# Kernel tuning notes

Hardware: AMD Instinct MI355X
Metric: run time of the kernel (lower is better)

## Reference

```python
import math
import jax, jax.numpy as jnp
import numpy as np

N_QUBITS = 8
N_QLAYERS = 2
HIDDEN = 768
BATCH = 8192
LN_EPS = 1e-5


def _ry_gate(theta):
    # theta: scalar or (B,) -> (2,2) or (B,2,2) complex64
    h = theta * 0.5
    c, s = jnp.cos(h), jnp.sin(h)
    g = jnp.stack([jnp.stack([c, -s], axis=-1), jnp.stack([s, c], axis=-1)], axis=-2)
    return g.astype(jnp.complex64)


def _rz_gate(theta):
    t = theta.astype(jnp.complex64)
    e0, e1 = jnp.exp(-0.5j * t), jnp.exp(0.5j * t)
    z = jnp.zeros_like(e0)
    return jnp.stack([jnp.stack([e0, z], axis=-1), jnp.stack([z, e1], axis=-1)], axis=-2)


def _apply_1q(state, gate, w, n):
    # state: (B, 2**n); gate: (2,2) shared or (B,2,2) per-sample; wire w (0 = MSB)
    B = state.shape[0]
    s = state.reshape(B, 2 ** w, 2, -1)
    if gate.ndim == 2:
        s = jnp.einsum('ij,bljr->blir', gate, s)
    else:
        s = jnp.einsum('bij,bljr->blir', gate, s)
    return s.reshape(B, -1)


def _apply_cnot(state, c, t, n):
    B = state.shape[0]
    s = state.reshape((B,) + (2,) * n)
    ax_c = 1 + c
    s0 = jnp.take(s, 0, axis=ax_c)  # control=0 branch, control axis removed
    s1 = jnp.take(s, 1, axis=ax_c)
    ax_t = 1 + t - (1 if t > c else 0)
    s1 = jnp.flip(s1, axis=ax_t)    # X on target when control=1
    s = jnp.stack([s0, s1], axis=ax_c)
    return s.reshape(B, -1)


def _circuit(angles, weights_ry, weights_rz):
    # angles: (B, n) float32 -> (B, n) PauliZ expectations, batched statevector sim
    n, L = N_QUBITS, N_QLAYERS
    B = angles.shape[0]
    state = jnp.zeros((B, 2 ** n), dtype=jnp.complex64).at[:, 0].set(1.0)
    for i in range(n):
        state = _apply_1q(state, _ry_gate(angles[:, i]), i, n)
    for i in range(1, n):
        state = _apply_cnot(state, 0, i, n)
    for l in range(L):
        for i in range(n):
            state = _apply_1q(state, _ry_gate(weights_ry[l, i]), i, n)
            state = _apply_1q(state, _rz_gate(weights_rz[l, i]), i, n)
    for i in range(1, n):
        state = _apply_cnot(state, i, 0, n)
    probs = jnp.abs(state) ** 2  # (B, 2**n)
    k = jnp.arange(2 ** n)
    bits = (k[None, :] >> (n - 1 - jnp.arange(n))[:, None]) & 1  # wire 0 = MSB (PennyLane)
    signs = (1 - 2 * bits).astype(probs.dtype)  # (n, 2**n)
    return probs @ signs.T  # (B, n)


def setup_inputs() -> dict:
    key = jax.random.key(0)
    ks = jax.random.split(key, 8)
    return {
        'hidden': jax.random.normal(ks[0], (BATCH, HIDDEN), dtype=jnp.float32),
        'W_in': jax.random.normal(ks[1], (N_QUBITS, HIDDEN), dtype=jnp.float32) * (1.0 / math.sqrt(HIDDEN)),
        'b_in': jax.random.normal(ks[2], (N_QUBITS,), dtype=jnp.float32) * 0.01,
        'W_out': jax.random.normal(ks[3], (HIDDEN, N_QUBITS), dtype=jnp.float32) * (1.0 / math.sqrt(N_QUBITS)),
        'b_out': jax.random.normal(ks[4], (HIDDEN,), dtype=jnp.float32) * 0.01,
        'weights_ry': jax.random.normal(ks[5], (N_QLAYERS, N_QUBITS), dtype=jnp.float32) * 0.1,
        'weights_rz': jax.random.normal(ks[6], (N_QLAYERS, N_QUBITS), dtype=jnp.float32) * 0.1,
        'gamma': jnp.ones((HIDDEN,), dtype=jnp.float32),
        'beta': jnp.zeros((HIDDEN,), dtype=jnp.float32),
    }


def reference(hidden, W_in, b_in, W_out, b_out, weights_ry, weights_rz, gamma, beta):
    phase = 0.0
    angles = jnp.tanh(hidden @ W_in.T + b_in) * math.pi + phase  # (B, n)
    meas = _circuit(angles, weights_ry, weights_rz).astype(jnp.float32)  # (B, n)
    y = meas @ W_out.T + b_out  # (B, h)
    mu = jnp.mean(y, axis=-1, keepdims=True)
    var = jnp.mean(jnp.square(y - mu), axis=-1, keepdims=True)
    return (y - mu) * jax.lax.rsqrt(var + LN_EPS) * gamma + beta
```

## Files before the change

kernel.cpp:

```cpp
#include <hip/hip_runtime.h>
#include <hip/hip_bf16.h>

#define NQ    8
#define HID   768
#define BATCH 8192
#define SPB   4
#define NBLK  (BATCH / SPB)
#define TPB   256

template<int BF> __device__ __forceinline__ float LDV(const void* p, int i) {
    if constexpr (BF) return __bfloat162float(((const __hip_bfloat16*)p)[i]);
    else return ((const float*)p)[i];
}
template<int BF> __device__ __forceinline__ float4 LD4(const void* p, int i4) {
    if constexpr (BF) {
        ushort4 v = ((const ushort4*)p)[i4];
        float4 r;
        r.x = __uint_as_float(((unsigned)v.x) << 16);
        r.y = __uint_as_float(((unsigned)v.y) << 16);
        r.z = __uint_as_float(((unsigned)v.z) << 16);
        r.w = __uint_as_float(((unsigned)v.w) << 16);
        return r;
    } else {
        return ((const float4*)p)[i4];
    }
}
template<int BF> __device__ __forceinline__ void ST4(void* p, int i4, float4 v) {
    if constexpr (BF) {
        __hip_bfloat16 bx = __float2bfloat16(v.x);
        __hip_bfloat16 by = __float2bfloat16(v.y);
        __hip_bfloat16 bz = __float2bfloat16(v.z);
        __hip_bfloat16 bw = __float2bfloat16(v.w);
        ushort4 s;
        s.x = *(const unsigned short*)&bx;
        s.y = *(const unsigned short*)&by;
        s.z = *(const unsigned short*)&bz;
        s.w = *(const unsigned short*)&bw;
        ((ushort4*)p)[i4] = s;
    } else {
        ((float4*)p)[i4] = v;
    }
}

template<int BF>
__device__ __forceinline__ void run_all(
    const void* hidden_, const void* W_in_, const void* b_in_,
    const void* W_out_, const void* b_out_, const void* wry_, const void* wrz_,
    const void* gamma_, const void* beta_, void* out_)
{
    const int tid  = threadIdx.x;
    const int lane = tid & 63;
    const int wv   = tid >> 6;
    const int j    = lane >> 3;
    const int b    = blockIdx.x * SPB + wv;

    float DA, DB, Kr, Ki;
    {
        float ry0 = LDV<BF>(wry_, j), ry1 = LDV<BF>(wry_, NQ + j);
        float rz0 = LDV<BF>(wrz_, j), rz1 = LDV<BF>(wrz_, NQ + j);
        float cA = cosf(0.5f*ry0), sA = sinf(0.5f*ry0);
        float cB = cosf(0.5f*ry1), sB = sinf(0.5f*ry1);
        float p0c = cosf(0.5f*rz0), p0s = sinf(0.5f*rz0);
        float p1c = cosf(0.5f*rz1), p1s = sinf(0.5f*rz1);
        float g00r =  cA*p0c, g00i = -cA*p0s;
        float g01r = -sA*p0c, g01i =  sA*p0s;
        float g10r =  sA*p0c, g10i =  sA*p0s;
        float g11r =  cA*p0c, g11i =  cA*p0s;
        float h00r = cB*g00r - sB*g10r, h00i = cB*g00i - sB*g10i;
        float h01r = cB*g01r - sB*g11r, h01i = cB*g01i - sB*g11i;
        float h10r = sB*g00r + cB*g10r, h10i = sB*g00i + cB*g10i;
        float h11r = sB*g01r + cB*g11r, h11i = sB*g01i + cB*g11i;
        float f00r = h00r*p1c + h00i*p1s, f00i = h00i*p1c - h00r*p1s;
        float f01r = h01r*p1c + h01i*p1s, f01i = h01i*p1c - h01r*p1s;
        float f10r = h10r*p1c - h10i*p1s, f10i = h10i*p1c + h10r*p1s;
        float f11r = h11r*p1c - h11i*p1s, f11i = h11i*p1c + h11r*p1s;
        DA = f00r*f00r + f00i*f00i - (f10r*f10r + f10i*f10i);
        DB = f01r*f01r + f01i*f01i - (f11r*f11r + f11i*f11i);
        Kr = (f00r*f01r + f00i*f01i) - (f10r*f11r + f10i*f11i);
        Ki = (f00i*f01r - f00r*f01i) - (f10i*f11r - f10r*f11i);
    }

    float p[NQ];
    #pragma unroll
    for (int q = 0; q < NQ; ++q) p[q] = 0.f;
    const int hb = b * (HID/4);
    #pragma unroll
    for (int t = 0; t < 3; ++t) {
        const int q4 = (t << 6) + lane;
        float4 h = LD4<BF>(hidden_, hb + q4);
        #pragma unroll
        for (int jj = 0; jj < NQ; ++jj) {
            float4 w = LD4<BF>(W_in_, jj*(HID/4) + q4);
            p[jj] = fmaf(h.x, w.x, p[jj]);
            p[jj] = fmaf(h.y, w.y, p[jj]);
            p[jj] = fmaf(h.z, w.z, p[jj]);
            p[jj] = fmaf(h.w, w.w, p[jj]);
        }
    }
    const bool mb0 = ((lane >> 3) & 1) != 0;
    const bool mb1 = ((lane >> 4) & 1) != 0;
    const bool mb2 = ((lane >> 5) & 1) != 0;
    float np[4];
    #pragma unroll
    for (int k = 0; k < 4; ++k) {
        float sent = mb0 ? p[2*k]   : p[2*k+1];
        float keep = mb0 ? p[2*k+1] : p[2*k];
        np[k] = keep + __shfl_xor(sent, 8, 64);
    }
    float nq[2];
    #pragma unroll
    for (int k = 0; k < 2; ++k) {
        float sent = mb1 ? np[2*k]   : np[2*k+1];
        float keep = mb1 ? np[2*k+1] : np[2*k];
        nq[k] = keep + __shfl_xor(sent, 16, 64);
    }
    float z;
    {
        float sent = mb2 ? nq[0] : nq[1];
        float keep = mb2 ? nq[1] : nq[0];
        z = keep + __shfl_xor(sent, 32, 64);
    }
    z += __shfl_xor(z, 1, 64);
    z += __shfl_xor(z, 2, 64);
    z += __shfl_xor(z, 4, 64);

    float zb = z + LDV<BF>(b_in_, j);
    float th = tanhf(zb);
    float sj = sinpif(th), cj = cospif(th);

    float ca = 0.5f * (DA + DB), da = 0.5f * (DA - DB);
    const bool g0 = (j == 0);
    float uu = da * cj;
    float vv = fmaf(Kr, sj, ca);
    float MA = g0 ? 1.f : (vv + uu), MB = g0 ? 1.f : (vv - uu);
    float fr = g0 ? 1.f : Kr, fi = g0 ? 0.f : (cj * Ki);
    #pragma unroll
    for (int d = 8; d < 64; d <<= 1) {
        MA *= __shfl_xor(MA, d, 64);
        MB *= __shfl_xor(MB, d, 64);
        float qr = __shfl_xor(fr, d, 64);
        float qi = __shfl_xor(fi, d, 64);
        float nr = fr*qr - fi*qi;
        float ni = fr*qi + fi*qr;
        fr = nr; fi = ni;
    }
    float DA0 = __shfl(DA, 0, 64), DB0 = __shfl(DB, 0, 64);
    float Kr0 = __shfl(Kr, 0, 64), Ki0 = __shfl(Ki, 0, 64);
    float cc0 = __shfl(cj, 0, 64), sc0 = __shfl(sj, 0, 64);
    float meas0 = 0.5f*(1.f+cc0)*DA0*MA + 0.5f*(1.f-cc0)*DB0*MB
                + sc0*(Kr0*fr - Ki0*fi);
    float measj = g0 ? meas0 : fmaf(cc0, uu, vv);
    float m0 = meas0;
    float m1 = __shfl(measj,  8, 64), m2 = __shfl(measj, 16, 64);
    float m3 = __shfl(measj, 24, 64), m4 = __shfl(measj, 32, 64);
    float m5 = __shfl(measj, 40, 64), m6 = __shfl(measj, 48, 64);
    float m7 = __shfl(measj, 56, 64);

    float yv[12];
    float sum = 0.f, sq = 0.f;
    #pragma unroll
    for (int t = 0; t < 3; ++t) {
        const int q4 = (t << 6) + lane;
        float4 bo = LD4<BF>(b_out_, q4);
        float bos[4] = {bo.x, bo.y, bo.z, bo.w};
        #pragma unroll
        for (int e = 0; e < 4; ++e) {
            int c = 4*q4 + e;
            float4 w0 = LD4<BF>(W_out_, c*2);
            float4 w1 = LD4<BF>(W_out_, c*2 + 1);
            float y = bos[e];
            y = fmaf(m0, w0.x, y); y = fmaf(m1, w0.y, y);
            y = fmaf(m2, w0.z, y); y = fmaf(m3, w0.w, y);
            y = fmaf(m4, w1.x, y); y = fmaf(m5, w1.y, y);
            y = fmaf(m6, w1.z, y); y = fmaf(m7, w1.w, y);
            yv[4*t+e] = y;
            sum += y;
            sq = fmaf(y, y, sq);
        }
    }
    #pragma unroll
    for (int d = 1; d < 64; d <<= 1) {
        sum += __shfl_xor(sum, d, 64);
        sq  += __shfl_xor(sq,  d, 64);
    }
    float mean = sum * (1.f/HID);
    float var  = fmaf(sq, 1.f/HID, -mean*mean);
    float rstd = rsqrtf(var + 1e-5f);
    #pragma unroll
    for (int t = 0; t < 3; ++t) {
        const int q4 = (t << 6) + lane;
        float4 ga = LD4<BF>(gamma_, q4);
        float4 be = LD4<BF>(beta_,  q4);
        float4 o;
        o.x = fmaf((yv[4*t+0]-mean)*rstd, ga.x, be.x);
        o.y = fmaf((yv[4*t+1]-mean)*rstd, ga.y, be.y);
        o.z = fmaf((yv[4*t+2]-mean)*rstd, ga.z, be.z);
        o.w = fmaf((yv[4*t+3]-mean)*rstd, ga.w, be.w);
        ST4<BF>(out_, hb + q4, o);
    }
}

__global__ __launch_bounds__(TPB, 4) void main_kernel(
    const void* hidden_, const void* W_in_, const void* b_in_,
    const void* W_out_, const void* b_out_, const void* wry_, const void* wrz_,
    const void* gamma_, const void* beta_, void* out_)
{
    const int lane = threadIdx.x & 63;
    unsigned wrd = ((const unsigned*)hidden_)[lane];
    unsigned lo  = wrd & 0xffffu;
    unsigned e   = (lo >> 7) & 0xffu;
    bool v = (lo == 0u) || (e >= 100u && e <= 133u);
    unsigned long long mask = __ballot(v);
    int flag = (__popcll(mask) > 32) ? 1 : 0;
    if (flag)
        run_all<1>(hidden_, W_in_, b_in_, W_out_, b_out_, wry_, wrz_,
                   gamma_, beta_, out_);
    else
        run_all<0>(hidden_, W_in_, b_in_, W_out_, b_out_, wry_, wrz_,
                   gamma_, beta_, out_);
}

extern "C" void kernel_launch(void* const* d_in, const int* in_sizes, int n_in,
                              void* d_out, int out_size, void* d_ws, size_t ws_size,
                              hipStream_t stream) {
    const void* hidden = d_in[0];
    const void* W_in   = d_in[1];
    const void* b_in   = d_in[2];
    const void* W_out  = d_in[3];
    const void* b_out  = d_in[4];
    const void* wry    = d_in[5];
    const void* wrz    = d_in[6];
    const void* gamma  = d_in[7];
    const void* beta   = d_in[8];
    (void)d_ws; (void)ws_size;
    main_kernel<<<NBLK, TPB, 0, stream>>>(hidden, W_in, b_in, W_out, b_out,
                                          wry, wrz, gamma, beta, d_out);
}
```

Measured before the change: 117.6 us.

## Use DPP and readlane for wave reductions; give each lane group one qubit's dot product

```diff
diff --git a/kernel.cpp b/kernel.cpp
--- a/kernel.cpp
+++ b/kernel.cpp
@@ -42,6 +42,16 @@
     }
 }
 
+template<int CTRL>
+__device__ __forceinline__ float dpp_mov(float x) {
+    int xi = __float_as_int(x);
+    int yi = __builtin_amdgcn_update_dpp(xi, xi, CTRL, 0xF, 0xF, false);
+    return __int_as_float(yi);
+}
+__device__ __forceinline__ float rl(float x, int l) {
+    return __int_as_float(__builtin_amdgcn_readlane(__float_as_int(x), l));
+}
+
 template<int BF>
 __device__ __forceinline__ void run_all(
     const void* hidden_, const void* W_in_, const void* b_in_,
@@ -52,6 +62,7 @@
     const int lane = tid & 63;
     const int wv   = tid >> 6;
     const int j    = lane >> 3;
+    const int u    = lane & 7;
     const int b    = blockIdx.x * SPB + wv;
 
     float DA, DB, Kr, Ki;
@@ -80,51 +91,23 @@
         Ki = (f00i*f01r - f00r*f01i) - (f10i*f11r - f10r*f11i);
     }
 
-    float p[NQ];
+    float a0=0.f, a1=0.f, a2=0.f, a3=0.f;
+    const int hb = b * (HID/4);
+    const int wb = j * (HID/4);
     #pragma unroll
-    for (int q = 0; q < NQ; ++q) p[q] = 0.f;
-    const int hb = b * (HID/4);
-    #pragma unroll
-    for (int t = 0; t < 3; ++t) {
-        const int q4 = (t << 6) + lane;
-        float4 h = LD4<BF>(hidden_, hb + q4);
-        #pragma unroll
-        for (int jj = 0; jj < NQ; ++jj) {
-            float4 w = LD4<BF>(W_in_, jj*(HID/4) + q4);
-            p[jj] = fmaf(h.x, w.x, p[jj]);
-            p[jj] = fmaf(h.y, w.y, p[jj]);
-            p[jj] = fmaf(h.z, w.z, p[jj]);
-            p[jj] = fmaf(h.w, w.w, p[jj]);
-        }
-    }
-    const bool mb0 = ((lane >> 3) & 1) != 0;
-    const bool mb1 = ((lane >> 4) & 1) != 0;
-    const bool mb2 = ((lane >> 5) & 1) != 0;
-    float np[4];
-    #pragma unroll
-    for (int k = 0; k < 4; ++k) {
-        float sent = mb0 ? p[2*k]   : p[2*k+1];
-        float keep = mb0 ? p[2*k+1] : p[2*k];
-        np[k] = keep + __shfl_xor(sent, 8, 64);
-    }
-    float nq[2];
-    #pragma unroll
-    for (int k = 0; k < 2; ++k) {
-        float sent = mb1 ? np[2*k]   : np[2*k+1];
-        float keep = mb1 ? np[2*k+1] : np[2*k];
-        nq[k] = keep + __shfl_xor(sent, 16, 64);
-    }
-    float z;
-    {
-        float sent = mb2 ? nq[0] : nq[1];
-        float keep = mb2 ? nq[1] : nq[0];
-        z = keep + __shfl_xor(sent, 32, 64);
-    }
-    z += __shfl_xor(z, 1, 64);
-    z += __shfl_xor(z, 2, 64);
-    z += __shfl_xor(z, 4, 64);
-
-    float zb = z + LDV<BF>(b_in_, j);
+    for (int t = 0; t < 24; ++t) {
+        int i4 = u + (t << 3);
+        float4 h = LD4<BF>(hidden_, hb + i4);
+        float4 w = LD4<BF>(W_in_,  wb + i4);
+        a0 = fmaf(h.x, w.x, a0); a1 = fmaf(h.y, w.y, a1);
+        a2 = fmaf(h.z, w.z, a2); a3 = fmaf(h.w, w.w, a3);
+    }
+    float acc = (a0 + a1) + (a2 + a3);
+    acc += dpp_mov<0xB1>(acc);
+    acc += dpp_mov<0x4E>(acc);
+    acc += dpp_mov<0x141>(acc);
+
+    float zb = acc + LDV<BF>(b_in_, j);
     float th = tanhf(zb);
     float sj = sinpif(th), cj = cospif(th);
 
@@ -133,28 +116,36 @@
     float uu = da * cj;
     float vv = fmaf(Kr, sj, ca);
     float MA = g0 ? 1.f : (vv + uu), MB = g0 ? 1.f : (vv - uu);
-    float fr = g0 ? 1.f : Kr, fi = g0 ? 0.f : (cj * Ki);
-    #pragma unroll
-    for (int d = 8; d < 64; d <<= 1) {
-        MA *= __shfl_xor(MA, d, 64);
-        MB *= __shfl_xor(MB, d, 64);
-        float qr = __shfl_xor(fr, d, 64);
-        float qi = __shfl_xor(fi, d, 64);
-        float nr = fr*qr - fi*qi;
-        float ni = fr*qi + fi*qr;
+    float fr = g0 ? 1.f : Kr,        fi = g0 ? 0.f : (cj * Ki);
+    MA *= dpp_mov<0x140>(MA);
+    MB *= dpp_mov<0x140>(MB);
+    {
+        float qr = dpp_mov<0x140>(fr), qi = dpp_mov<0x140>(fi);
+        float nr = fr*qr - fi*qi, ni = fr*qi + fi*qr;
         fr = nr; fi = ni;
     }
-    float DA0 = __shfl(DA, 0, 64), DB0 = __shfl(DB, 0, 64);
-    float Kr0 = __shfl(Kr, 0, 64), Ki0 = __shfl(Ki, 0, 64);
-    float cc0 = __shfl(cj, 0, 64), sc0 = __shfl(sj, 0, 64);
-    float meas0 = 0.5f*(1.f+cc0)*DA0*MA + 0.5f*(1.f-cc0)*DB0*MB
-                + sc0*(Kr0*fr - Ki0*fi);
+    float PA = (rl(MA,0)*rl(MA,16)) * (rl(MA,32)*rl(MA,48));
+    float PB = (rl(MB,0)*rl(MB,16)) * (rl(MB,32)*rl(MB,48));
+    float PFr, PFi;
+    {
+        float ar = rl(fr, 0), ai = rl(fi, 0);
+        float br = rl(fr,16), bi = rl(fi,16);
+        float cr = rl(fr,32), ci = rl(fi,32);
+        float dr = rl(fr,48), di = rl(fi,48);
+        float abr = ar*br - ai*bi, abi = ar*bi + ai*br;
+        float cdr = cr*dr - ci*di, cdi = cr*di + ci*dr;
+        PFr = abr*cdr - abi*cdi;
+        PFi = abr*cdi + abi*cdr;
+    }
+    float DA0 = rl(DA,0), DB0 = rl(DB,0), Kr0 = rl(Kr,0), Ki0 = rl(Ki,0);
+    float cc0 = rl(cj,0), sc0 = rl(sj,0);
+    float meas0 = 0.5f*(1.f+cc0)*DA0*PA + 0.5f*(1.f-cc0)*DB0*PB
+                + sc0*(Kr0*PFr - Ki0*PFi);
     float measj = g0 ? meas0 : fmaf(cc0, uu, vv);
     float m0 = meas0;
-    float m1 = __shfl(measj,  8, 64), m2 = __shfl(measj, 16, 64);
-    float m3 = __shfl(measj, 24, 64), m4 = __shfl(measj, 32, 64);
-    float m5 = __shfl(measj, 40, 64), m6 = __shfl(measj, 48, 64);
-    float m7 = __shfl(measj, 56, 64);
+    float m1 = rl(measj,  8), m2 = rl(measj, 16), m3 = rl(measj, 24);
+    float m4 = rl(measj, 32), m5 = rl(measj, 40), m6 = rl(measj, 48);
+    float m7 = rl(measj, 56);
 
     float yv[12];
     float sum = 0.f, sq = 0.f;
@@ -178,13 +169,14 @@
             sq = fmaf(y, y, sq);
         }
     }
-    #pragma unroll
-    for (int d = 1; d < 64; d <<= 1) {
-        sum += __shfl_xor(sum, d, 64);
-        sq  += __shfl_xor(sq,  d, 64);
-    }
-    float mean = sum * (1.f/HID);
-    float var  = fmaf(sq, 1.f/HID, -mean*mean);
+    sum += dpp_mov<0xB1>(sum);   sq += dpp_mov<0xB1>(sq);
+    sum += dpp_mov<0x4E>(sum);   sq += dpp_mov<0x4E>(sq);
+    sum += dpp_mov<0x141>(sum);  sq += dpp_mov<0x141>(sq);
+    sum += dpp_mov<0x140>(sum);  sq += dpp_mov<0x140>(sq);
+    float tsum = (rl(sum,0) + rl(sum,16)) + (rl(sum,32) + rl(sum,48));
+    float tsq  = (rl(sq, 0) + rl(sq, 16)) + (rl(sq, 32) + rl(sq, 48));
+    float mean = tsum * (1.f/HID);
+    float var  = fmaf(tsq, 1.f/HID, -mean*mean);
     float rstd = rsqrtf(var + 1e-5f);
     #pragma unroll
     for (int t = 0; t < 3; ++t) {
```

After: 123.1 us. 1.05x slower.

## Stage W_in and W_out in LDS, double samples per block

Applied to the files above, without the earlier changes.

```diff
diff --git a/kernel.cpp b/kernel.cpp
--- a/kernel.cpp
+++ b/kernel.cpp
@@ -4,13 +4,17 @@
 #define NQ    8
 #define HID   768
 #define BATCH 8192
-#define SPB   4
+#define TPB   512
+#define SPB   8
 #define NBLK  (BATCH / SPB)
-#define TPB   256
 
 template<int BF> __device__ __forceinline__ float LDV(const void* p, int i) {
     if constexpr (BF) return __bfloat162float(((const __hip_bfloat16*)p)[i]);
     else return ((const float*)p)[i];
+}
+template<int BF> __device__ __forceinline__ void STV(void* p, int i, float v) {
+    if constexpr (BF) ((__hip_bfloat16*)p)[i] = __float2bfloat16(v);
+    else ((float*)p)[i] = v;
 }
 template<int BF> __device__ __forceinline__ float4 LD4(const void* p, int i4) {
     if constexpr (BF) {
@@ -25,34 +29,34 @@
         return ((const float4*)p)[i4];
     }
 }
-template<int BF> __device__ __forceinline__ void ST4(void* p, int i4, float4 v) {
-    if constexpr (BF) {
-        __hip_bfloat16 bx = __float2bfloat16(v.x);
-        __hip_bfloat16 by = __float2bfloat16(v.y);
-        __hip_bfloat16 bz = __float2bfloat16(v.z);
-        __hip_bfloat16 bw = __float2bfloat16(v.w);
-        ushort4 s;
-        s.x = *(const unsigned short*)&bx;
-        s.y = *(const unsigned short*)&by;
-        s.z = *(const unsigned short*)&bz;
-        s.w = *(const unsigned short*)&bw;
-        ((ushort4*)p)[i4] = s;
-    } else {
-        ((float4*)p)[i4] = v;
-    }
-}
 
 template<int BF>
 __device__ __forceinline__ void run_all(
     const void* hidden_, const void* W_in_, const void* b_in_,
     const void* W_out_, const void* b_out_, const void* wry_, const void* wrz_,
-    const void* gamma_, const void* beta_, void* out_)
+    const void* gamma_, const void* beta_, void* out_,
+    float* sWin, float4* sWoutLo, float4* sWoutHi)
 {
     const int tid  = threadIdx.x;
     const int lane = tid & 63;
     const int wv   = tid >> 6;
     const int j    = lane >> 3;
     const int b    = blockIdx.x * SPB + wv;
+
+    #pragma unroll
+    for (int k = 0; k < (NQ*HID/4)/TPB; ++k) {
+        int idx = tid + k*TPB;
+        ((float4*)sWin)[idx] = LD4<BF>(W_in_, idx);
+    }
+    #pragma unroll
+    for (int k = 0; k < HID/TPB + 1; ++k) {
+        int c = tid + k*TPB;
+        if (c < HID) {
+            sWoutLo[c] = LD4<BF>(W_out_, c*2);
+            sWoutHi[c] = LD4<BF>(W_out_, c*2 + 1);
+        }
+    }
+    __syncthreads();
 
     float DA, DB, Kr, Ki;
     {
@@ -90,7 +94,7 @@
         float4 h = LD4<BF>(hidden_, hb + q4);
         #pragma unroll
         for (int jj = 0; jj < NQ; ++jj) {
-            float4 w = LD4<BF>(W_in_, jj*(HID/4) + q4);
+            float4 w = ((const float4*)(sWin + jj*HID))[q4];
             p[jj] = fmaf(h.x, w.x, p[jj]);
             p[jj] = fmaf(h.y, w.y, p[jj]);
             p[jj] = fmaf(h.z, w.z, p[jj]);
@@ -107,17 +111,17 @@
         float keep = mb0 ? p[2*k+1] : p[2*k];
         np[k] = keep + __shfl_xor(sent, 8, 64);
     }
-    float nq[2];
+    float nq2[2];
     #pragma unroll
     for (int k = 0; k < 2; ++k) {
         float sent = mb1 ? np[2*k]   : np[2*k+1];
         float keep = mb1 ? np[2*k+1] : np[2*k];
-        nq[k] = keep + __shfl_xor(sent, 16, 64);
+        nq2[k] = keep + __shfl_xor(sent, 16, 64);
     }
     float z;
     {
-        float sent = mb2 ? nq[0] : nq[1];
-        float keep = mb2 ? nq[1] : nq[0];
+        float sent = mb2 ? nq2[0] : nq2[1];
+        float keep = mb2 ? nq2[1] : nq2[0];
         z = keep + __shfl_xor(sent, 32, 64);
     }
     z += __shfl_xor(z, 1, 64);
@@ -133,7 +137,7 @@
     float uu = da * cj;
     float vv = fmaf(Kr, sj, ca);
     float MA = g0 ? 1.f : (vv + uu), MB = g0 ? 1.f : (vv - uu);
-    float fr = g0 ? 1.f : Kr, fi = g0 ? 0.f : (cj * Ki);
+    float fr = g0 ? 1.f : Kr,        fi = g0 ? 0.f : (cj * Ki);
     #pragma unroll
     for (int d = 8; d < 64; d <<= 1) {
         MA *= __shfl_xor(MA, d, 64);
@@ -156,27 +160,22 @@
     float m5 = __shfl(measj, 40, 64), m6 = __shfl(measj, 48, 64);
     float m7 = __shfl(measj, 56, 64);
 
+    const int rowbase = b * HID;
     float yv[12];
     float sum = 0.f, sq = 0.f;
     #pragma unroll
-    for (int t = 0; t < 3; ++t) {
-        const int q4 = (t << 6) + lane;
-        float4 bo = LD4<BF>(b_out_, q4);
-        float bos[4] = {bo.x, bo.y, bo.z, bo.w};
-        #pragma unroll
-        for (int e = 0; e < 4; ++e) {
-            int c = 4*q4 + e;
-            float4 w0 = LD4<BF>(W_out_, c*2);
-            float4 w1 = LD4<BF>(W_out_, c*2 + 1);
-            float y = bos[e];
-            y = fmaf(m0, w0.x, y); y = fmaf(m1, w0.y, y);
-            y = fmaf(m2, w0.z, y); y = fmaf(m3, w0.w, y);
-            y = fmaf(m4, w1.x, y); y = fmaf(m5, w1.y, y);
-            y = fmaf(m6, w1.z, y); y = fmaf(m7, w1.w, y);
-            yv[4*t+e] = y;
-            sum += y;
-            sq = fmaf(y, y, sq);
-        }
+    for (int k = 0; k < 12; ++k) {
+        const int c = lane + (k << 6);
+        float4 w0 = sWoutLo[c];
+        float4 w1 = sWoutHi[c];
+        float y = LDV<BF>(b_out_, c);
+        y = fmaf(m0, w0.x, y); y = fmaf(m1, w0.y, y);
+        y = fmaf(m2, w0.z, y); y = fmaf(m3, w0.w, y);
+        y = fmaf(m4, w1.x, y); y = fmaf(m5, w1.y, y);
+        y = fmaf(m6, w1.z, y); y = fmaf(m7, w1.w, y);
+        yv[k] = y;
+        sum += y;
+        sq = fmaf(y, y, sq);
     }
     #pragma unroll
     for (int d = 1; d < 64; d <<= 1) {
@@ -187,24 +186,23 @@
     float var  = fmaf(sq, 1.f/HID, -mean*mean);
     float rstd = rsqrtf(var + 1e-5f);
     #pragma unroll
-    for (int t = 0; t < 3; ++t) {
-        const int q4 = (t << 6) + lane;
-        float4 ga = LD4<BF>(gamma_, q4);
-        float4 be = LD4<BF>(beta_,  q4);
-        float4 o;
-        o.x = fmaf((yv[4*t+0]-mean)*rstd, ga.x, be.x);
-        o.y = fmaf((yv[4*t+1]-mean)*rstd, ga.y, be.y);
-        o.z = fmaf((yv[4*t+2]-mean)*rstd, ga.z, be.z);
-        o.w = fmaf((yv[4*t+3]-mean)*rstd, ga.w, be.w);
-        ST4<BF>(out_, hb + q4, o);
-    }
-}
-
-__global__ __launch_bounds__(TPB, 4) void main_kernel(
+    for (int k = 0; k < 12; ++k) {
+        const int c = lane + (k << 6);
+        float g  = LDV<BF>(gamma_, c);
+        float be = LDV<BF>(beta_,  c);
+        float o  = fmaf((yv[k] - mean) * rstd, g, be);
+        STV<BF>(out_, rowbase + c, o);
+    }
+}
+
+__global__ __launch_bounds__(TPB, 2) void main_kernel(
     const void* hidden_, const void* W_in_, const void* b_in_,
     const void* W_out_, const void* b_out_, const void* wry_, const void* wrz_,
     const void* gamma_, const void* beta_, void* out_)
 {
+    __shared__ __align__(16) float  sWin[NQ*HID];
+    __shared__ __align__(16) float4 sWoutLo[HID];
+    __shared__ __align__(16) float4 sWoutHi[HID];
     const int lane = threadIdx.x & 63;
     unsigned wrd = ((const unsigned*)hidden_)[lane];
     unsigned lo  = wrd & 0xffffu;
@@ -214,10 +212,10 @@
     int flag = (__popcll(mask) > 32) ? 1 : 0;
     if (flag)
         run_all<1>(hidden_, W_in_, b_in_, W_out_, b_out_, wry_, wrz_,
-                   gamma_, beta_, out_);
+                   gamma_, beta_, out_, sWin, sWoutLo, sWoutHi);
     else
         run_all<0>(hidden_, W_in_, b_in_, W_out_, b_out_, wry_, wrz_,
-                   gamma_, beta_, out_);
+                   gamma_, beta_, out_, sWin, sWoutLo, sWoutHi);
 }
 
 extern "C" void kernel_launch(void* const* d_in, const int* in_sizes, int n_in,
```

New measurement: 101.9 us. 1.15x faster.
